# Kernel tuning notes

Measured on AMD Instinct MI355X. Metric: run time of the kernel, lower is better.

The kernel has to match this reference:

```python
import jax, jax.numpy as jnp
import numpy as np

V, E, H = 32000, 128, 256
B, S, T = 32, 128, 128


def lstm(emb, Wih, Whh, bih, bhh, h0, c0):
    """Single-layer batch_first LSTM matching torch.nn.LSTM (gate order i,f,g,o).
    emb: [B,T,E] -> (outputs [B,T,H], h_T [B,H], c_T [B,H])."""
    b = bih + bhh  # [4H]
    xg = jnp.einsum('bte,ge->btg', emb, Wih) + b  # precompute input gates [B,T,4H]

    def step(carry, xg_t):
        h, c = carry
        gates = xg_t + h @ Whh.T  # [B,4H]
        i, f, g, o = jnp.split(gates, 4, axis=-1)
        i, f, o = jax.nn.sigmoid(i), jax.nn.sigmoid(f), jax.nn.sigmoid(o)
        g = jnp.tanh(g)
        c = f * c + i * g
        h = o * jnp.tanh(c)
        return (h, c), h

    (hT, cT), hs = jax.lax.scan(step, (h0, c0), jnp.swapaxes(xg, 0, 1))
    return jnp.swapaxes(hs, 0, 1), hT, cT


def setup_inputs() -> dict:
    key = jax.random.key(0)
    ks = jax.random.split(key, 14)
    s_e, s_h = 1.0 / np.sqrt(H), 1.0 / np.sqrt(H)
    return {
        'x': jax.random.randint(ks[0], (B, S), 0, V),
        'y': jax.random.randint(ks[1], (B, T), 0, V),
        'enc_emb': jax.random.normal(ks[2], (V, E), jnp.float32),
        'dec_emb': jax.random.normal(ks[3], (V, E), jnp.float32),
        'Wih_enc': jax.random.uniform(ks[4], (4 * H, E), jnp.float32, -s_e, s_e),
        'Whh_enc': jax.random.uniform(ks[5], (4 * H, H), jnp.float32, -s_h, s_h),
        'bih_enc': jax.random.uniform(ks[6], (4 * H,), jnp.float32, -s_h, s_h),
        'bhh_enc': jax.random.uniform(ks[7], (4 * H,), jnp.float32, -s_h, s_h),
        'Wih_dec': jax.random.uniform(ks[8], (4 * H, E), jnp.float32, -s_e, s_e),
        'Whh_dec': jax.random.uniform(ks[9], (4 * H, H), jnp.float32, -s_h, s_h),
        'bih_dec': jax.random.uniform(ks[10], (4 * H,), jnp.float32, -s_h, s_h),
        'bhh_dec': jax.random.uniform(ks[11], (4 * H,), jnp.float32, -s_h, s_h),
        'W_out': jax.random.uniform(ks[12], (V, H), jnp.float32, -s_h, s_h),
        'b_out': jax.random.uniform(ks[13], (V,), jnp.float32, -s_h, s_h),
    }


def reference(x, y, enc_emb, dec_emb, Wih_enc, Whh_enc, bih_enc, bhh_enc,
              Wih_dec, Whh_dec, bih_dec, bhh_dec, W_out, b_out):
    h0 = jnp.zeros((x.shape[0], H), jnp.float32)
    c0 = jnp.zeros((x.shape[0], H), jnp.float32)
    # encoder
    x_emb = enc_emb[x]  # [B,S,E]
    _, h, c = lstm(x_emb, Wih_enc, Whh_enc, bih_enc, bhh_enc, h0, c0)
    # decoder (teacher forcing)
    y_emb = dec_emb[y]  # [B,T,E]
    dec_out, _, _ = lstm(y_emb, Wih_dec, Whh_dec, bih_dec, bhh_dec, h, c)
    logits = jnp.einsum('bth,vh->btv', dec_out, W_out) + b_out  # [B,T,V]
    return logits
```

## Files before the change

kernel.cpp:

```cpp
#include <hip/hip_runtime.h>


typedef _Float16 half2v __attribute__((ext_vector_type(2)));
typedef short bf16x8 __attribute__((ext_vector_type(8)));
typedef float f32x4 __attribute__((ext_vector_type(4)));

__device__ __forceinline__ unsigned short f2h_bits(float f) {
  _Float16 h = (_Float16)f;
  return __builtin_bit_cast(unsigned short, h);
}

__device__ __forceinline__ unsigned short f2bf_bits(float f) {
  unsigned u = __builtin_bit_cast(unsigned, f);
  u += 0x7fffu + ((u >> 16) & 1u);
  return (unsigned short)(u >> 16);
}

__device__ __forceinline__ float fdot2u(unsigned wu, unsigned hu, float acc) {
#if defined(__has_builtin) && __has_builtin(__builtin_amdgcn_fdot2)
  return __builtin_amdgcn_fdot2(__builtin_bit_cast(half2v, wu),
                                __builtin_bit_cast(half2v, hu), acc, false);
#else
  half2v a = __builtin_bit_cast(half2v, wu);
  half2v b = __builtin_bit_cast(half2v, hu);
  return acc + (float)a[0] * (float)b[0] + (float)a[1] * (float)b[1];
#endif
}

__device__ __forceinline__ float tanh_fast(float x) {
  float e = __expf(2.f * x);
  return 1.f - 2.f / (e + 1.f);
}

__device__ __forceinline__ float sigmoid_fast(float x) {
  return 1.f / (1.f + __expf(-x));
}

__device__ __forceinline__ void gload_lds16(const void* g, void* l) {
#if defined(__has_builtin) && __has_builtin(__builtin_amdgcn_global_load_lds)
  __builtin_amdgcn_global_load_lds(
      (const __attribute__((address_space(1))) void*)g,
      (__attribute__((address_space(3))) void*)l, 16, 0, 0);
#else
  *(uint4*)l = *(const uint4*)g;
#endif
}

__global__ void prep_kernel(const float* __restrict__ WhhE, const float* __restrict__ WhhD,
                            const float* __restrict__ Wout,
                            unsigned* __restrict__ WhhP, unsigned short* __restrict__ WoutB) {
  int i = blockIdx.x * blockDim.x + threadIdx.x;
  int stride = gridDim.x * blockDim.x;
  for (int idx = i; idx < 262144; idx += stride) {
    int p = idx >> 17;
    int rem = idx & 131071;
    int d = rem >> 10;
    int g = rem & 1023;
    const float* W = p ? WhhD : WhhE;
    float a = W[g * 256 + 2 * d];
    float b = W[g * 256 + 2 * d + 1];
    WhhP[idx] = (unsigned)f2h_bits(a) | ((unsigned)f2h_bits(b) << 16);
  }
  for (int idx = i; idx < 8192000; idx += stride) {
    WoutB[idx] = f2bf_bits(Wout[idx]);
  }
}

__global__ __launch_bounds__(256, 2) void xg_kernel(
    const int* __restrict__ x, const int* __restrict__ y,
    const float* __restrict__ enc_emb, const float* __restrict__ dec_emb,
    const float* __restrict__ Wih_enc, const float* __restrict__ Wih_dec,
    float* __restrict__ xg) {
  __shared__ float Al[64][132];
  __shared__ float Bl[64][132];
  __shared__ int tok[64];
  const int nb = blockIdx.x;
  const int mbb = blockIdx.y;
  const int m0 = mbb * 64;
  const int p = mbb >> 6;
  const int tid = threadIdx.x;

  if (tid < 64) {
    int mloc = (m0 + tid) & 4095;
    tok[tid] = p ? y[mloc] : x[mloc];
  }
  __syncthreads();

  const float* emb = p ? dec_emb : enc_emb;
  const float* Wih = p ? Wih_dec : Wih_enc;
  {
    int ri = tid & 63, seg = tid >> 6;
    const float* er = emb + (size_t)tok[ri] * 128 + seg * 32;
    const float* wr = Wih + (size_t)(nb * 64 + ri) * 128 + seg * 32;
#pragma unroll
    for (int c = 0; c < 8; ++c) {
      *(float4*)&Al[ri][seg * 32 + c * 4] = *(const float4*)&er[c * 4];
      *(float4*)&Bl[ri][seg * 32 + c * 4] = *(const float4*)&wr[c * 4];
    }
  }
  __syncthreads();

  const int tx = tid & 15, ty = tid >> 4;
  float acc[4][4];
#pragma unroll
  for (int mm = 0; mm < 4; ++mm)
#pragma unroll
    for (int nn = 0; nn < 4; ++nn) acc[mm][nn] = 0.f;

  for (int k4 = 0; k4 < 32; ++k4) {
    float4 av[4], bv[4];
#pragma unroll
    for (int mm = 0; mm < 4; ++mm) av[mm] = *(const float4*)&Al[mm * 16 + ty][k4 * 4];
#pragma unroll
    for (int nn = 0; nn < 4; ++nn) bv[nn] = *(const float4*)&Bl[nn * 16 + tx][k4 * 4];
#pragma unroll
    for (int mm = 0; mm < 4; ++mm)
#pragma unroll
      for (int nn = 0; nn < 4; ++nn) {
        acc[mm][nn] = fmaf(av[mm].x, bv[nn].x, acc[mm][nn]);
        acc[mm][nn] = fmaf(av[mm].y, bv[nn].y, acc[mm][nn]);
        acc[mm][nn] = fmaf(av[mm].z, bv[nn].z, acc[mm][nn]);
        acc[mm][nn] = fmaf(av[mm].w, bv[nn].w, acc[mm][nn]);
      }
  }
#pragma unroll
  for (int mm = 0; mm < 4; ++mm)
#pragma unroll
    for (int nn = 0; nn < 4; ++nn)
      xg[(size_t)(m0 + mm * 16 + ty) * 1024 + nb * 64 + nn * 16 + tx] = acc[mm][nn];
}

__global__ __launch_bounds__(1024, 1) void lstm_kernel(
    const float* __restrict__ xg, const unsigned* __restrict__ WhhP,
    const float* __restrict__ bih_enc, const float* __restrict__ bhh_enc,
    const float* __restrict__ bih_dec, const float* __restrict__ bhh_dec,
    unsigned short* __restrict__ decO) {
  const int b = blockIdx.x;
  const int t = threadIdx.x;
  const int g = t;
  const int q = t >> 8;
  const int j = t & 255;

  __shared__ __align__(16) unsigned h2[128];
  __shared__ float gact[4][256];
  __shared__ unsigned WL[18 * 2048];

  if (t < 128) h2[t] = 0u;
  float c_r = 0.f;
  __syncthreads();

  unsigned wqd[92];
  float bias_g = 0.f;

  float xgv_n = xg[(size_t)(b << 7) * 1024 + g];

  for (int s = 0; s < 256; ++s) {
    const int p = s >> 7;
    const int tt = s & 127;

    if ((s & 127) == 0) {
      const unsigned* base = WhhP + (p << 17);
#pragma unroll
      for (int d = 0; d < 92; ++d) wqd[d] = base[(d << 10) + g];
#pragma unroll
      for (int dd = 0; dd < 36; ++dd)
        WL[((dd >> 1) << 11) + (g << 1) + (dd & 1)] = base[((92 + dd) << 10) + g];
      bias_g = p ? (bih_dec[g] + bhh_dec[g]) : (bih_enc[g] + bhh_enc[g]);
    }

    const float xgv = xgv_n;
    if (s < 255) {
      const int sn = s + 1;
      xgv_n = xg[(size_t)(((sn >> 7) << 12) + (b << 7) + (sn & 127)) * 1024 + g];
    }

    float a0 = 0.f, a1 = 0.f, a2 = 0.f, a3 = 0.f;
#pragma unroll
    for (int c = 0; c < 23; ++c) {
      const uint4 hv = *(const uint4*)&h2[c << 2];
      a0 = fdot2u(wqd[4 * c + 0], hv.x, a0);
      a1 = fdot2u(wqd[4 * c + 1], hv.y, a1);
      a2 = fdot2u(wqd[4 * c + 2], hv.z, a2);
      a3 = fdot2u(wqd[4 * c + 3], hv.w, a3);
    }
#pragma unroll
    for (int c = 23; c < 32; ++c) {
      const uint4 hv = *(const uint4*)&h2[c << 2];
      const int dp0 = (4 * c - 92) >> 1;
      const uint2 w01 = *(const uint2*)&WL[(dp0 << 11) + (g << 1)];
      const uint2 w23 = *(const uint2*)&WL[((dp0 + 1) << 11) + (g << 1)];
      a0 = fdot2u(w01.x, hv.x, a0);
      a1 = fdot2u(w01.y, hv.y, a1);
      a2 = fdot2u(w23.x, hv.z, a2);
      a3 = fdot2u(w23.y, hv.w, a3);
    }
    const float accf = bias_g + xgv + ((a0 + a1) + (a2 + a3));

    const float act = (q == 2) ? tanh_fast(accf) : sigmoid_fast(accf);
    gact[q][j] = act;
    __syncthreads();

    if (t < 256) {
      const float iv = gact[0][t];
      const float fv = gact[1][t];
      const float gv = gact[2][t];
      const float ov = gact[3][t];
      c_r = fv * c_r + iv * gv;
      const float hh = ov * tanh_fast(c_r);
      if (p) decO[(size_t)((b << 7) + tt) * 256 + t] = f2bf_bits(hh);
      const float hn = __shfl_down(hh, 1, 64);
      if (!(t & 1))
        h2[t >> 1] = (unsigned)f2h_bits(hh) | ((unsigned)f2h_bits(hn) << 16);
    }
    __syncthreads();
  }
}

__global__ __launch_bounds__(256, 2) void proj_kernel(
    const unsigned short* __restrict__ A,
    const unsigned short* __restrict__ Bw,
    const float* __restrict__ bias, float* __restrict__ out) {
  __shared__ unsigned short Bl[64 * 256];
  __shared__ unsigned short Al[2][32 * 256];
  const int n0 = blockIdx.x << 6;
  const int tid = threadIdx.x;
  const int wv = tid >> 6, ln = tid & 63;
  const int wm = wv & 1;
  const int wn = wv >> 1;
  const int l16 = ln & 15, lq = ln >> 4;

#pragma unroll
  for (int it = 0; it < 8; ++it) {
    int st = it * 256 + tid;
    int m = st >> 5, k8 = st & 31;
    gload_lds16(Bw + (size_t)(n0 + m) * 256 + ((k8 ^ (m & 15)) << 3), &Bl[st << 3]);
  }
#pragma unroll
  for (int it = 0; it < 4; ++it) {
    int st = it * 256 + tid;
    int m = st >> 5, k8 = st & 31;
    gload_lds16(A + (size_t)m * 256 + ((k8 ^ (m & 15)) << 3), &Al[0][st << 3]);
  }
  asm volatile("s_waitcnt vmcnt(0)" ::: "memory");
  __syncthreads();

  bf16x8 bfr[2][8];
#pragma unroll
  for (int nt = 0; nt < 2; ++nt)
#pragma unroll
    for (int ks = 0; ks < 8; ++ks) {
      int n = (wn << 5) + (nt << 4) + l16;
      int k8 = (ks << 2) + lq;
      bfr[nt][ks] = *(const bf16x8*)&Bl[((n << 5) | (k8 ^ (n & 15))) << 3];
    }
  const int gc0 = n0 + (wn << 5) + l16;
  const float bs0 = bias[gc0];
  const float bs1 = bias[gc0 + 16];

  for (int c = 0; c < 128; ++c) {
    const int cur = c & 1;
    if (c < 127) {
      const unsigned short* Ab = A + (size_t)(c + 1) * (32 * 256);
#pragma unroll
      for (int it = 0; it < 4; ++it) {
        int st = it * 256 + tid;
        int m = st >> 5, k8 = st & 31;
        gload_lds16(Ab + (size_t)m * 256 + ((k8 ^ (m & 15)) << 3), &Al[cur ^ 1][st << 3]);
      }
    }

    f32x4 acc0 = {}, acc1 = {};
#pragma unroll
    for (int ks = 0; ks < 8; ++ks) {
      const int k8 = (ks << 2) + lq;
      const int m = (wm << 4) + l16;
      const bf16x8 af = *(const bf16x8*)&Al[cur][((m << 5) | (k8 ^ (m & 15))) << 3];
      acc0 = __builtin_amdgcn_mfma_f32_16x16x32_bf16(af, bfr[0][ks], acc0, 0, 0, 0);
      acc1 = __builtin_amdgcn_mfma_f32_16x16x32_bf16(af, bfr[1][ks], acc1, 0, 0, 0);
    }

    const int grow0 = (c << 5) + (wm << 4) + (lq << 2);
#pragma unroll
    for (int rr = 0; rr < 4; ++rr) {
      out[(size_t)(grow0 + rr) * 32000 + gc0] = acc0[rr] + bs0;
      out[(size_t)(grow0 + rr) * 32000 + gc0 + 16] = acc1[rr] + bs1;
    }

    asm volatile("s_waitcnt vmcnt(8)" ::: "memory");
    __syncthreads();
  }
}

extern "C" void kernel_launch(void* const* d_in, const int* in_sizes, int n_in,
                              void* d_out, int out_size, void* d_ws, size_t ws_size,
                              hipStream_t stream) {
  const int* x = (const int*)d_in[0];
  const int* y = (const int*)d_in[1];
  const float* enc_emb = (const float*)d_in[2];
  const float* dec_emb = (const float*)d_in[3];
  const float* Wih_enc = (const float*)d_in[4];
  const float* Whh_enc = (const float*)d_in[5];
  const float* bih_enc = (const float*)d_in[6];
  const float* bhh_enc = (const float*)d_in[7];
  const float* Wih_dec = (const float*)d_in[8];
  const float* Whh_dec = (const float*)d_in[9];
  const float* bih_dec = (const float*)d_in[10];
  const float* bhh_dec = (const float*)d_in[11];
  const float* W_out = (const float*)d_in[12];
  const float* b_out = (const float*)d_in[13];

  char* ws = (char*)d_ws;
  float* xg = (float*)ws;
  unsigned* WhhP = (unsigned*)(ws + 33554432);
  unsigned short* WoutB = (unsigned short*)(ws + 34603008);
  unsigned short* decO = (unsigned short*)(ws + 50987008);
  if (ws_size < 57344000) return;

  prep_kernel<<<4096, 256, 0, stream>>>(Whh_enc, Whh_dec, W_out, WhhP, WoutB);
  xg_kernel<<<dim3(16, 128), 256, 0, stream>>>(x, y, enc_emb, dec_emb, Wih_enc, Wih_dec, xg);
  lstm_kernel<<<32, 1024, 0, stream>>>(xg, WhhP, bih_enc, bhh_enc, bih_dec, bhh_dec, decO);
  proj_kernel<<<500, 256, 0, stream>>>(decO, WoutB, b_out, (float*)d_out);
}
```

Before: 1.282 ms.

## Interleave LSTM gates across lanes with shuffles and stage projection stores through LDS

The LSTM kernel remaps threads so the four gates of each hidden unit sit in adjacent lanes. Gate values are now exchanged with wave shuffles instead of a shared gact array, and the h buffer is double-buffered. This removes one block-wide barrier and an LDS round trip from each of the 256 serial steps, and computes sigmoid and tanh through one branch-free formula. The projection kernel writes each 32x64 output tile into padded LDS and then stores it as coalesced float4 rows, relaxing the vmcnt wait. That costs an extra barrier per tile, and the 66-float row pitch leaves odd rows not 16-byte aligned for the float4 LDS reads.

```diff
diff --git a/kernel.cpp b/kernel.cpp
--- a/kernel.cpp
+++ b/kernel.cpp
@@ -30,10 +30,6 @@
 __device__ __forceinline__ float tanh_fast(float x) {
   float e = __expf(2.f * x);
   return 1.f - 2.f / (e + 1.f);
-}
-
-__device__ __forceinline__ float sigmoid_fast(float x) {
-  return 1.f / (1.f + __expf(-x));
 }
 
 __device__ __forceinline__ void gload_lds16(const void* g, void* l) {
@@ -137,34 +133,36 @@
     unsigned short* __restrict__ decO) {
   const int b = blockIdx.x;
   const int t = threadIdx.x;
-  const int g = t;
-  const int q = t >> 8;
-  const int j = t & 255;
-
-  __shared__ __align__(16) unsigned h2[128];
-  __shared__ float gact[4][256];
+  const int qc = t & 3;
+  const int u = t >> 2;
+  const int g = (qc << 8) + u;
+
+  __shared__ __align__(16) unsigned h2[2][128];
   __shared__ unsigned WL[18 * 2048];
 
-  if (t < 128) h2[t] = 0u;
+  if (t < 128) h2[0][t] = 0u;
   float c_r = 0.f;
   __syncthreads();
 
   unsigned wqd[92];
   float bias_g = 0.f;
+  const float s_act = (qc == 2) ? 2.f : 1.f;
+  const float o_act = 1.f - s_act;
 
   float xgv_n = xg[(size_t)(b << 7) * 1024 + g];
 
   for (int s = 0; s < 256; ++s) {
     const int p = s >> 7;
     const int tt = s & 127;
-
-    if ((s & 127) == 0) {
+    const int rb = s & 1;
+
+    if (tt == 0) {
       const unsigned* base = WhhP + (p << 17);
 #pragma unroll
       for (int d = 0; d < 92; ++d) wqd[d] = base[(d << 10) + g];
 #pragma unroll
       for (int dd = 0; dd < 36; ++dd)
-        WL[((dd >> 1) << 11) + (g << 1) + (dd & 1)] = base[((92 + dd) << 10) + g];
+        WL[((dd >> 1) << 11) + (t << 1) + (dd & 1)] = base[((92 + dd) << 10) + g];
       bias_g = p ? (bih_dec[g] + bhh_dec[g]) : (bih_enc[g] + bhh_enc[g]);
     }
 
@@ -177,7 +175,7 @@
     float a0 = 0.f, a1 = 0.f, a2 = 0.f, a3 = 0.f;
 #pragma unroll
     for (int c = 0; c < 23; ++c) {
-      const uint4 hv = *(const uint4*)&h2[c << 2];
+      const uint4 hv = *(const uint4*)&h2[rb][c << 2];
       a0 = fdot2u(wqd[4 * c + 0], hv.x, a0);
       a1 = fdot2u(wqd[4 * c + 1], hv.y, a1);
       a2 = fdot2u(wqd[4 * c + 2], hv.z, a2);
@@ -185,10 +183,10 @@
     }
 #pragma unroll
     for (int c = 23; c < 32; ++c) {
-      const uint4 hv = *(const uint4*)&h2[c << 2];
+      const uint4 hv = *(const uint4*)&h2[rb][c << 2];
       const int dp0 = (4 * c - 92) >> 1;
-      const uint2 w01 = *(const uint2*)&WL[(dp0 << 11) + (g << 1)];
-      const uint2 w23 = *(const uint2*)&WL[((dp0 + 1) << 11) + (g << 1)];
+      const uint2 w01 = *(const uint2*)&WL[(dp0 << 11) + (t << 1)];
+      const uint2 w23 = *(const uint2*)&WL[((dp0 + 1) << 11) + (t << 1)];
       a0 = fdot2u(w01.x, hv.x, a0);
       a1 = fdot2u(w01.y, hv.y, a1);
       a2 = fdot2u(w23.x, hv.z, a2);
@@ -196,22 +194,26 @@
     }
     const float accf = bias_g + xgv + ((a0 + a1) + (a2 + a3));
 
-    const float act = (q == 2) ? tanh_fast(accf) : sigmoid_fast(accf);
-    gact[q][j] = act;
-    __syncthreads();
-
-    if (t < 256) {
-      const float iv = gact[0][t];
-      const float fv = gact[1][t];
-      const float gv = gact[2][t];
-      const float ov = gact[3][t];
-      c_r = fv * c_r + iv * gv;
-      const float hh = ov * tanh_fast(c_r);
-      if (p) decO[(size_t)((b << 7) + tt) * 256 + t] = f2bf_bits(hh);
-      const float hn = __shfl_down(hh, 1, 64);
-      if (!(t & 1))
-        h2[t >> 1] = (unsigned)f2h_bits(hh) | ((unsigned)f2h_bits(hn) << 16);
-    }
+    const float e = __expf(-s_act * accf);
+    const float act = fmaf(s_act, 1.f / (1.f + e), o_act);
+
+    const float pv = __shfl_xor(act, 1, 64);
+    const float lo = (qc & 1) ? pv : act;
+    const float hi = (qc & 1) ? act : pv;
+    const float lo2 = __shfl_xor(lo, 2, 64);
+    const float hi2 = __shfl_xor(hi, 2, 64);
+    const bool m2 = (qc & 2) != 0;
+    const float iv = m2 ? lo2 : lo;
+    const float fv = m2 ? hi2 : hi;
+    const float gv = m2 ? lo : lo2;
+    const float ov = m2 ? hi : hi2;
+
+    c_r = fv * c_r + iv * gv;
+    const float hh = ov * tanh_fast(c_r);
+    if (p && qc == 0) decO[(size_t)((b << 7) + tt) * 256 + u] = f2bf_bits(hh);
+    const float hn = __shfl_down(hh, 4, 64);
+    if ((t & 7) == 0)
+      h2[rb ^ 1][t >> 3] = (unsigned)f2h_bits(hh) | ((unsigned)f2h_bits(hn) << 16);
     __syncthreads();
   }
 }
@@ -222,6 +224,7 @@
     const float* __restrict__ bias, float* __restrict__ out) {
   __shared__ unsigned short Bl[64 * 256];
   __shared__ unsigned short Al[2][32 * 256];
+  __shared__ float Ol[32][66];
   const int n0 = blockIdx.x << 6;
   const int tid = threadIdx.x;
   const int wv = tid >> 6, ln = tid & 63;
@@ -253,9 +256,9 @@
       int k8 = (ks << 2) + lq;
       bfr[nt][ks] = *(const bf16x8*)&Bl[((n << 5) | (k8 ^ (n & 15))) << 3];
     }
-  const int gc0 = n0 + (wn << 5) + l16;
-  const float bs0 = bias[gc0];
-  const float bs1 = bias[gc0 + 16];
+  const int gc0 = (wn << 5) + l16;
+  const float bs0 = bias[n0 + gc0];
+  const float bs1 = bias[n0 + gc0 + 16];
 
   for (int c = 0; c < 128; ++c) {
     const int cur = c & 1;
@@ -279,14 +282,23 @@
       acc1 = __builtin_amdgcn_mfma_f32_16x16x32_bf16(af, bfr[1][ks], acc1, 0, 0, 0);
     }
 
-    const int grow0 = (c << 5) + (wm << 4) + (lq << 2);
+    const int orow = (wm << 4) + (lq << 2);
 #pragma unroll
     for (int rr = 0; rr < 4; ++rr) {
-      out[(size_t)(grow0 + rr) * 32000 + gc0] = acc0[rr] + bs0;
-      out[(size_t)(grow0 + rr) * 32000 + gc0 + 16] = acc1[rr] + bs1;
-    }
-
-    asm volatile("s_waitcnt vmcnt(8)" ::: "memory");
+      Ol[orow + rr][gc0] = acc0[rr] + bs0;
+      Ol[orow + rr][gc0 + 16] = acc1[rr] + bs1;
+    }
+    __syncthreads();
+
+#pragma unroll
+    for (int pp = 0; pp < 2; ++pp) {
+      const int r = (pp << 4) + (tid >> 4);
+      const int sl = tid & 15;
+      const float4 v = *(const float4*)&Ol[r][sl << 2];
+      *(float4*)&out[(size_t)((c << 5) + r) * 32000 + n0 + (sl << 2)] = v;
+    }
+
+    asm volatile("s_waitcnt vmcnt(2)" ::: "memory");
     __syncthreads();
   }
 }
```

Result: slower. 1.333 ms (+3.9%).
